# Kernel optimization log

Hardware: AMD Instinct MI355X
Metric: run time of the kernel (lower is better)

The kernel has to match this reference:

```python
import jax, jax.numpy as jnp
import numpy as np

T, B, X, Y = 24, 16, 64, 64
S, M, C = 16, 8, 8
F = S + M + C   # GRU input_size = 32
H = 32          # hidden_size


def setup_inputs() -> dict:
    key = jax.random.key(0)
    ks = jax.random.split(key, 8)
    inv = 1.0 / np.sqrt(H)
    return {
        "spatial": jax.random.normal(ks[0], (T, B, X, Y, S), dtype=jnp.float32),
        "meteorology": jax.random.normal(ks[1], (T, B, X, Y, M), dtype=jnp.float32),
        "context": jax.random.normal(ks[2], (T, B, X, Y, C), dtype=jnp.float32),
        # GRU parameters (torch layout: [3H, F] and [3H, H], gate order r,z,n)
        "W_ih": jax.random.uniform(ks[3], (3 * H, F), jnp.float32, -inv, inv),
        "W_hh": jax.random.uniform(ks[4], (3 * H, H), jnp.float32, -inv, inv),
        "b_ih": jax.random.uniform(ks[5], (3 * H,), jnp.float32, -inv, inv),
        "b_hh": jax.random.uniform(ks[6], (3 * H,), jnp.float32, -inv, inv),
        # output projection (hidden -> spatial_size)
        "W": jax.random.normal(ks[7], (H, S), dtype=jnp.float32),
    }


def reference(spatial, meteorology, context, W_ih, W_hh, b_ih, b_hh, W):
    # cat features: (T, B, X, Y, F); merge all pixels + batch into one GRU batch
    x = jnp.concatenate((spatial, meteorology, context), axis=4)
    N = B * X * Y
    x = x.reshape(T, N, F)

    # precompute input projections for all timesteps: (T, N, 3H)
    gx_all = jnp.einsum('tnf,gf->tng', x, W_ih) + b_ih

    def step(h, gx):
        gh = h @ W_hh.T + b_hh                      # (N, 3H)
        r = jax.nn.sigmoid(gx[:, :H] + gh[:, :H])
        z = jax.nn.sigmoid(gx[:, H:2 * H] + gh[:, H:2 * H])
        n = jnp.tanh(gx[:, 2 * H:] + r * gh[:, 2 * H:])
        h = (1.0 - z) * n + z * h
        return h, None

    h0 = jnp.zeros((N, H), dtype=x.dtype)
    h_final, _ = jax.lax.scan(step, h0, gx_all)     # (N, H)

    out = h_final @ W                               # (N, S)
    return out.reshape(B, X, Y, S)
```

## Files before the change

### kernel.cpp

```cpp
#include <hip/hip_runtime.h>
#include <hip/hip_bf16.h>


#define TSTEPS 24
#define NPIX 65536
#define PADW 40

typedef __attribute__((ext_vector_type(8))) short bf16x8;
typedef __attribute__((ext_vector_type(4))) float f32x4;
typedef __attribute__((ext_vector_type(4))) unsigned int u32x4;

#define MFMA16(a, b, c) __builtin_amdgcn_mfma_f32_16x16x32_bf16((a), (b), (c), 0, 0, 0)

#define SCL_RZ (-1.4426950408889634f)
#define SCL_N  ( 2.8853900817779268f)

__device__ __forceinline__ unsigned short f2bf(float f) {
  unsigned u = __builtin_bit_cast(unsigned, f);
  u += 0x7fffu + ((u >> 16) & 1u);
  return (unsigned short)(u >> 16);
}

__device__ __forceinline__ unsigned pk2(float a, float b) {
  __hip_bfloat162 h = __float22bfloat162_rn(float2{a, b});
  unsigned u;
  __builtin_memcpy(&u, &h, sizeof(u));
  return u;
}

__device__ __forceinline__ bf16x8 pack8(f32x4 a, f32x4 b) {
  u32x4 r = { pk2(a[0], a[1]), pk2(a[2], a[3]), pk2(b[0], b[1]), pk2(b[2], b[3]) };
  return __builtin_bit_cast(bf16x8, r);
}

__device__ __forceinline__ float sig2(float t) {
  return __builtin_amdgcn_rcpf(1.f + __builtin_amdgcn_exp2f(t));
}
__device__ __forceinline__ float tanh2(float t) {
  return 1.f - 2.f * __builtin_amdgcn_rcpf(1.f + __builtin_amdgcn_exp2f(t));
}

__device__ __forceinline__ int tau(int k) {
  int q = k >> 3, j = k & 7;
  return (j < 4) ? (q * 4 + j) : (16 + q * 4 + (j - 4));
}

__global__ __launch_bounds__(256, 2)
void gru_fused(const float* __restrict__ spatial, const float* __restrict__ met,
               const float* __restrict__ ctx,
               const float* __restrict__ W_ih, const float* __restrict__ W_hh,
               const float* __restrict__ b_ih, const float* __restrict__ b_hh,
               const float* __restrict__ Wout, float* __restrict__ out) {
  __shared__ __align__(16) unsigned short sW[192 * PADW];
  __shared__ __align__(16) float sCB[64];
  __shared__ __align__(16) float sBIN[32];
  __shared__ __align__(16) float sBHN[32];

  const int tid = threadIdx.x;
  for (int i = tid; i < 96 * 32; i += 256) {
    int r = i >> 5, c = i & 31;
    float s = (r < 64) ? SCL_RZ : SCL_N;
    sW[r * PADW + c] = f2bf(W_ih[i] * s);
    sW[(96 + r) * PADW + c] = f2bf(W_hh[r * 32 + tau(c)] * s);
  }
  if (tid < 64) sCB[tid] = (b_ih[tid] + b_hh[tid]) * SCL_RZ;
  else if (tid < 96) sBIN[tid - 64] = b_ih[tid] * SCL_N;
  else if (tid < 128) sBHN[tid - 96] = b_hh[tid - 32] * SCL_N;
  __syncthreads();

  const int lane = tid & 63;
  const int col = lane & 15;
  const int q = lane >> 4;
  const int wave = blockIdx.x * 4 + (tid >> 6);
  const long p0 = (long)wave * 32 + col;
  const long p1 = p0 + 16;

  f32x4 cS[4];
#pragma unroll
  for (int i = 0; i < 4; ++i) cS[i] = *(const f32x4*)&sCB[i * 16 + q * 4];
  const f32x4 cG4 = *(const f32x4*)&sBIN[q * 4];
  const f32x4 cG5 = *(const f32x4*)&sBIN[16 + q * 4];
  const f32x4 cH4 = *(const f32x4*)&sBHN[q * 4];
  const f32x4 cH5 = *(const f32x4*)&sBHN[16 + q * 4];

  const int wb = col * PADW + q * 8;
  const bf16x8 a0 = *(const bf16x8*)&sW[wb];
  const bf16x8 a1 = *(const bf16x8*)&sW[wb + 16 * PADW];
  const bf16x8 a2 = *(const bf16x8*)&sW[wb + 32 * PADW];
  const bf16x8 a3 = *(const bf16x8*)&sW[wb + 48 * PADW];
  const bf16x8 a4 = *(const bf16x8*)&sW[wb + 64 * PADW];
  const bf16x8 a5 = *(const bf16x8*)&sW[wb + 80 * PADW];
  const bf16x8 w0 = *(const bf16x8*)&sW[wb + 96 * PADW];
  const bf16x8 w1 = *(const bf16x8*)&sW[wb + 112 * PADW];
  const bf16x8 w2 = *(const bf16x8*)&sW[wb + 128 * PADW];
  const bf16x8 w3 = *(const bf16x8*)&sW[wb + 144 * PADW];
  const bf16x8 w4 = *(const bf16x8*)&sW[wb + 160 * PADW];
  const bf16x8 w5 = *(const bf16x8*)&sW[wb + 176 * PADW];

  const float *xp0, *xp1;
  long xstride;
  if (q < 2) {
    xp0 = spatial + p0 * 16 + q * 8; xp1 = spatial + p1 * 16 + q * 8;
    xstride = (long)NPIX * 16;
  } else if (q == 2) {
    xp0 = met + p0 * 8; xp1 = met + p1 * 8; xstride = (long)NPIX * 8;
  } else {
    xp0 = ctx + p0 * 8; xp1 = ctx + p1 * 8; xstride = (long)NPIX * 8;
  }

  bf16x8 bx0 = pack8(*(const f32x4*)xp0, *(const f32x4*)(xp0 + 4));
  bf16x8 bx1 = pack8(*(const f32x4*)xp1, *(const f32x4*)(xp1 + 4));
  xp0 += xstride; xp1 += xstride;

  f32x4 h0a = {0.f, 0.f, 0.f, 0.f}, h0b = {0.f, 0.f, 0.f, 0.f};
  f32x4 h1a = {0.f, 0.f, 0.f, 0.f}, h1b = {0.f, 0.f, 0.f, 0.f};
  const f32x4 zero = {0.f, 0.f, 0.f, 0.f};

#pragma unroll 1
  for (int t = 0; t < TSTEPS; ++t) {
    f32x4 xn0a, xn0b, xn1a, xn1b;
    if (t < TSTEPS - 1) {
      xn0a = *(const f32x4*)xp0; xn0b = *(const f32x4*)(xp0 + 4);
      xn1a = *(const f32x4*)xp1; xn1b = *(const f32x4*)(xp1 + 4);
      xp0 += xstride; xp1 += xstride;
    }

    bf16x8 bh0 = pack8(h0a, h0b);
    bf16x8 bh1 = pack8(h1a, h1b);

    f32x4 G00 = MFMA16(a0, bx0, cS[0]);  f32x4 G10 = MFMA16(a0, bx1, cS[0]);
    f32x4 G01 = MFMA16(a1, bx0, cS[1]);  f32x4 G11 = MFMA16(a1, bx1, cS[1]);
    f32x4 G02 = MFMA16(a2, bx0, cS[2]);  f32x4 G12 = MFMA16(a2, bx1, cS[2]);
    f32x4 G03 = MFMA16(a3, bx0, cS[3]);  f32x4 G13 = MFMA16(a3, bx1, cS[3]);
    f32x4 G04 = MFMA16(a4, bx0, cG4);    f32x4 G14 = MFMA16(a4, bx1, cG4);
    f32x4 G05 = MFMA16(a5, bx0, cG5);    f32x4 G15 = MFMA16(a5, bx1, cG5);

    f32x4 R00 = MFMA16(w0, bh0, G00);    f32x4 R10 = MFMA16(w0, bh1, G10);
    f32x4 R01 = MFMA16(w1, bh0, G01);    f32x4 R11 = MFMA16(w1, bh1, G11);
    f32x4 Z00 = MFMA16(w2, bh0, G02);    f32x4 Z10 = MFMA16(w2, bh1, G12);
    f32x4 Z01 = MFMA16(w3, bh0, G03);    f32x4 Z11 = MFMA16(w3, bh1, G13);
    f32x4 H04 = MFMA16(w4, bh0, cH4);    f32x4 H14 = MFMA16(w4, bh1, cH4);
    f32x4 H05 = MFMA16(w5, bh0, cH5);    f32x4 H15 = MFMA16(w5, bh1, cH5);

#pragma unroll
    for (int r = 0; r < 4; ++r) {
      float r00 = sig2(R00[r]);
      float r01 = sig2(R01[r]);
      float z00 = sig2(Z00[r]);
      float z01 = sig2(Z01[r]);
      float n00 = tanh2(__builtin_fmaf(r00, H04[r], G04[r]));
      float n01 = tanh2(__builtin_fmaf(r01, H05[r], G05[r]));
      h0a[r] = n00 + z00 * (h0a[r] - n00);
      h0b[r] = n01 + z01 * (h0b[r] - n01);

      float r10 = sig2(R10[r]);
      float r11 = sig2(R11[r]);
      float z10 = sig2(Z10[r]);
      float z11 = sig2(Z11[r]);
      float n10 = tanh2(__builtin_fmaf(r10, H14[r], G14[r]));
      float n11 = tanh2(__builtin_fmaf(r11, H15[r], G15[r]));
      h1a[r] = n10 + z10 * (h1a[r] - n10);
      h1b[r] = n11 + z11 * (h1b[r] - n11);
    }

    if (t < TSTEPS - 1) {
      bx0 = pack8(xn0a, xn0b);
      bx1 = pack8(xn1a, xn1b);
    }
  }

  bf16x8 bhf0 = pack8(h0a, h0b);
  bf16x8 bhf1 = pack8(h1a, h1b);
  float w[8];
#pragma unroll
  for (int j = 0; j < 8; ++j) {
    int tk = (j < 4) ? (q * 4 + j) : (16 + q * 4 + (j - 4));
    w[j] = Wout[tk * 16 + col];
  }
  u32x4 awp = { pk2(w[0], w[1]), pk2(w[2], w[3]), pk2(w[4], w[5]), pk2(w[6], w[7]) };
  bf16x8 aw = __builtin_bit_cast(bf16x8, awp);
  f32x4 o0 = MFMA16(aw, bhf0, zero);
  f32x4 o1 = MFMA16(aw, bhf1, zero);
  *(f32x4*)&out[p0 * 16 + q * 4] = o0;
  *(f32x4*)&out[p1 * 16 + q * 4] = o1;
}

extern "C" void kernel_launch(void* const* d_in, const int* in_sizes, int n_in,
                              void* d_out, int out_size, void* d_ws, size_t ws_size,
                              hipStream_t stream) {
  const float* spatial = (const float*)d_in[0];
  const float* met     = (const float*)d_in[1];
  const float* ctx     = (const float*)d_in[2];
  const float* W_ih    = (const float*)d_in[3];
  const float* W_hh    = (const float*)d_in[4];
  const float* b_ih    = (const float*)d_in[5];
  const float* b_hh    = (const float*)d_in[6];
  const float* Wout    = (const float*)d_in[7];
  float* out = (float*)d_out;

  gru_fused<<<dim3(NPIX / 32 / 4), dim3(256), 0, stream>>>(
      spatial, met, ctx, W_ih, W_hh, b_ih, b_hh, Wout, out);
}
```

Baseline: 230.3 us.

## Stream GRU inputs through a per-wave LDS ring using async global-to-LDS loads

Input loading moves from a one-step-ahead register prefetch to `global_load_lds` copies into a three-slab LDS ring private to each wave. This keeps two timesteps of input in flight, using explicit `vmcnt` waits and a loop unrolled in groups of three. The goal is to hide global memory latency in a kernel that reads inputs at a modest rate because each wave walks sequentially through timesteps. The cost is about 48 KB of extra LDS per block, which could limit occupancy, plus an added LDS read on every step.

```diff
diff --git a/kernel.cpp b/kernel.cpp
--- a/kernel.cpp
+++ b/kernel.cpp
@@ -5,6 +5,7 @@
 #define TSTEPS 24
 #define NPIX 65536
 #define PADW 40
+#define RING_STEP 16384
 
 typedef __attribute__((ext_vector_type(8))) short bf16x8;
 typedef __attribute__((ext_vector_type(4))) float f32x4;
@@ -44,6 +45,9 @@
   int q = k >> 3, j = k & 7;
   return (j < 4) ? (q * 4 + j) : (16 + q * 4 + (j - 4));
 }
+
+#define AS1 __attribute__((address_space(1)))
+#define AS3 __attribute__((address_space(3)))
 
 __global__ __launch_bounds__(256, 2)
 void gru_fused(const float* __restrict__ spatial, const float* __restrict__ met,
@@ -51,6 +55,7 @@
                const float* __restrict__ W_ih, const float* __restrict__ W_hh,
                const float* __restrict__ b_ih, const float* __restrict__ b_hh,
                const float* __restrict__ Wout, float* __restrict__ out) {
+  __shared__ __align__(16) unsigned char ring[3 * RING_STEP];
   __shared__ __align__(16) unsigned short sW[192 * PADW];
   __shared__ __align__(16) float sCB[64];
   __shared__ __align__(16) float sBIN[32];
@@ -71,7 +76,8 @@
   const int lane = tid & 63;
   const int col = lane & 15;
   const int q = lane >> 4;
-  const int wave = blockIdx.x * 4 + (tid >> 6);
+  const int wv = tid >> 6;
+  const int wave = blockIdx.x * 4 + wv;
   const long p0 = (long)wave * 32 + col;
   const long p1 = p0 + 16;
 
@@ -108,66 +114,83 @@
     xp0 = ctx + p0 * 8; xp1 = ctx + p1 * 8; xstride = (long)NPIX * 8;
   }
 
-  bf16x8 bx0 = pack8(*(const f32x4*)xp0, *(const f32x4*)(xp0 + 4));
-  bf16x8 bx1 = pack8(*(const f32x4*)xp1, *(const f32x4*)(xp1 + 4));
-  xp0 += xstride; xp1 += xstride;
+#define ISSUE_X(SLAB)                                                          \
+  do {                                                                         \
+    unsigned char* lb = &ring[(SLAB) * RING_STEP + wv * 4096];                 \
+    __builtin_amdgcn_global_load_lds((const AS1 unsigned int*)xp0,             \
+                                     (AS3 unsigned int*)(lb), 16, 0, 0);       \
+    __builtin_amdgcn_global_load_lds((const AS1 unsigned int*)(xp0 + 4),       \
+                                     (AS3 unsigned int*)(lb + 1024), 16, 0, 0);\
+    __builtin_amdgcn_global_load_lds((const AS1 unsigned int*)xp1,             \
+                                     (AS3 unsigned int*)(lb + 2048), 16, 0, 0);\
+    __builtin_amdgcn_global_load_lds((const AS1 unsigned int*)(xp1 + 4),       \
+                                     (AS3 unsigned int*)(lb + 3072), 16, 0, 0);\
+    xp0 += xstride; xp1 += xstride;                                            \
+  } while (0)
 
   f32x4 h0a = {0.f, 0.f, 0.f, 0.f}, h0b = {0.f, 0.f, 0.f, 0.f};
   f32x4 h1a = {0.f, 0.f, 0.f, 0.f}, h1b = {0.f, 0.f, 0.f, 0.f};
   const f32x4 zero = {0.f, 0.f, 0.f, 0.f};
 
+#define STEPW(RS, WS, DOLOAD, WAIT)                                            \
+  do {                                                                         \
+    if (DOLOAD) ISSUE_X(WS);                                                   \
+    asm volatile("s_waitcnt " WAIT ::: "memory");                              \
+    __builtin_amdgcn_sched_barrier(0);                                         \
+    const unsigned char* rb = &ring[(RS) * RING_STEP + wv * 4096 + lane * 16]; \
+    f32x4 x0a = *(const f32x4*)(rb);                                           \
+    f32x4 x0b = *(const f32x4*)(rb + 1024);                                    \
+    f32x4 x1a = *(const f32x4*)(rb + 2048);                                    \
+    f32x4 x1b = *(const f32x4*)(rb + 3072);                                    \
+    bf16x8 bx0 = pack8(x0a, x0b);                                              \
+    bf16x8 bx1 = pack8(x1a, x1b);                                              \
+    bf16x8 bh0 = pack8(h0a, h0b);                                              \
+    bf16x8 bh1 = pack8(h1a, h1b);                                              \
+    f32x4 G00 = MFMA16(a0, bx0, cS[0]);  f32x4 G10 = MFMA16(a0, bx1, cS[0]);   \
+    f32x4 G01 = MFMA16(a1, bx0, cS[1]);  f32x4 G11 = MFMA16(a1, bx1, cS[1]);   \
+    f32x4 G02 = MFMA16(a2, bx0, cS[2]);  f32x4 G12 = MFMA16(a2, bx1, cS[2]);   \
+    f32x4 G03 = MFMA16(a3, bx0, cS[3]);  f32x4 G13 = MFMA16(a3, bx1, cS[3]);   \
+    f32x4 G04 = MFMA16(a4, bx0, cG4);    f32x4 G14 = MFMA16(a4, bx1, cG4);     \
+    f32x4 G05 = MFMA16(a5, bx0, cG5);    f32x4 G15 = MFMA16(a5, bx1, cG5);     \
+    f32x4 R00 = MFMA16(w0, bh0, G00);    f32x4 R10 = MFMA16(w0, bh1, G10);     \
+    f32x4 R01 = MFMA16(w1, bh0, G01);    f32x4 R11 = MFMA16(w1, bh1, G11);     \
+    f32x4 Z00 = MFMA16(w2, bh0, G02);    f32x4 Z10 = MFMA16(w2, bh1, G12);     \
+    f32x4 Z01 = MFMA16(w3, bh0, G03);    f32x4 Z11 = MFMA16(w3, bh1, G13);     \
+    f32x4 H04 = MFMA16(w4, bh0, cH4);    f32x4 H14 = MFMA16(w4, bh1, cH4);     \
+    f32x4 H05 = MFMA16(w5, bh0, cH5);    f32x4 H15 = MFMA16(w5, bh1, cH5);     \
+    _Pragma("unroll")                                                          \
+    for (int r = 0; r < 4; ++r) {                                              \
+      float r00 = sig2(R00[r]);                                                \
+      float r01 = sig2(R01[r]);                                                \
+      float z00 = sig2(Z00[r]);                                                \
+      float z01 = sig2(Z01[r]);                                                \
+      float n00 = tanh2(__builtin_fmaf(r00, H04[r], G04[r]));                  \
+      float n01 = tanh2(__builtin_fmaf(r01, H05[r], G05[r]));                  \
+      h0a[r] = n00 + z00 * (h0a[r] - n00);                                     \
+      h0b[r] = n01 + z01 * (h0b[r] - n01);                                     \
+      float r10 = sig2(R10[r]);                                                \
+      float r11 = sig2(R11[r]);                                                \
+      float z10 = sig2(Z10[r]);                                                \
+      float z11 = sig2(Z11[r]);                                                \
+      float n10 = tanh2(__builtin_fmaf(r10, H14[r], G14[r]));                  \
+      float n11 = tanh2(__builtin_fmaf(r11, H15[r], G15[r]));                  \
+      h1a[r] = n10 + z10 * (h1a[r] - n10);                                     \
+      h1b[r] = n11 + z11 * (h1b[r] - n11);                                     \
+    }                                                                          \
+  } while (0)
+
+  ISSUE_X(0);
+  ISSUE_X(1);
+
 #pragma unroll 1
-  for (int t = 0; t < TSTEPS; ++t) {
-    f32x4 xn0a, xn0b, xn1a, xn1b;
-    if (t < TSTEPS - 1) {
-      xn0a = *(const f32x4*)xp0; xn0b = *(const f32x4*)(xp0 + 4);
-      xn1a = *(const f32x4*)xp1; xn1b = *(const f32x4*)(xp1 + 4);
-      xp0 += xstride; xp1 += xstride;
-    }
-
-    bf16x8 bh0 = pack8(h0a, h0b);
-    bf16x8 bh1 = pack8(h1a, h1b);
-
-    f32x4 G00 = MFMA16(a0, bx0, cS[0]);  f32x4 G10 = MFMA16(a0, bx1, cS[0]);
-    f32x4 G01 = MFMA16(a1, bx0, cS[1]);  f32x4 G11 = MFMA16(a1, bx1, cS[1]);
-    f32x4 G02 = MFMA16(a2, bx0, cS[2]);  f32x4 G12 = MFMA16(a2, bx1, cS[2]);
-    f32x4 G03 = MFMA16(a3, bx0, cS[3]);  f32x4 G13 = MFMA16(a3, bx1, cS[3]);
-    f32x4 G04 = MFMA16(a4, bx0, cG4);    f32x4 G14 = MFMA16(a4, bx1, cG4);
-    f32x4 G05 = MFMA16(a5, bx0, cG5);    f32x4 G15 = MFMA16(a5, bx1, cG5);
-
-    f32x4 R00 = MFMA16(w0, bh0, G00);    f32x4 R10 = MFMA16(w0, bh1, G10);
-    f32x4 R01 = MFMA16(w1, bh0, G01);    f32x4 R11 = MFMA16(w1, bh1, G11);
-    f32x4 Z00 = MFMA16(w2, bh0, G02);    f32x4 Z10 = MFMA16(w2, bh1, G12);
-    f32x4 Z01 = MFMA16(w3, bh0, G03);    f32x4 Z11 = MFMA16(w3, bh1, G13);
-    f32x4 H04 = MFMA16(w4, bh0, cH4);    f32x4 H14 = MFMA16(w4, bh1, cH4);
-    f32x4 H05 = MFMA16(w5, bh0, cH5);    f32x4 H15 = MFMA16(w5, bh1, cH5);
-
-#pragma unroll
-    for (int r = 0; r < 4; ++r) {
-      float r00 = sig2(R00[r]);
-      float r01 = sig2(R01[r]);
-      float z00 = sig2(Z00[r]);
-      float z01 = sig2(Z01[r]);
-      float n00 = tanh2(__builtin_fmaf(r00, H04[r], G04[r]));
-      float n01 = tanh2(__builtin_fmaf(r01, H05[r], G05[r]));
-      h0a[r] = n00 + z00 * (h0a[r] - n00);
-      h0b[r] = n01 + z01 * (h0b[r] - n01);
-
-      float r10 = sig2(R10[r]);
-      float r11 = sig2(R11[r]);
-      float z10 = sig2(Z10[r]);
-      float z11 = sig2(Z11[r]);
-      float n10 = tanh2(__builtin_fmaf(r10, H14[r], G14[r]));
-      float n11 = tanh2(__builtin_fmaf(r11, H15[r], G15[r]));
-      h1a[r] = n10 + z10 * (h1a[r] - n10);
-      h1b[r] = n11 + z11 * (h1b[r] - n11);
-    }
-
-    if (t < TSTEPS - 1) {
-      bx0 = pack8(xn0a, xn0b);
-      bx1 = pack8(xn1a, xn1b);
-    }
-  }
+  for (int tt = 0; tt < 7; ++tt) {
+    STEPW(0, 2, true, "vmcnt(8)");
+    STEPW(1, 0, true, "vmcnt(8)");
+    STEPW(2, 1, true, "vmcnt(8)");
+  }
+  STEPW(0, 2, true,  "vmcnt(8)");
+  STEPW(1, 0, false, "vmcnt(4)");
+  STEPW(2, 1, false, "vmcnt(0)");
 
   bf16x8 bhf0 = pack8(h0a, h0b);
   bf16x8 bhf1 = pack8(h1a, h1b);
```

Result: slower. 237.5 us (+3.1%).
